# Optimization experiments

Measured on AMD Instinct MI355X. Metric: run time of the kernel, lower is better.

## Reference

```python
import jax, jax.numpy as jnp
import numpy as np

D_MODEL = 1024
N_HEADS = 16
HEAD_DIM = D_MODEL // N_HEADS
NEG_INF = -1e9


def setup_inputs() -> dict:
    key = jax.random.key(0)
    ks = jax.random.split(key, 12)
    B, S = 2, 2048
    std = 1.0 / np.sqrt(D_MODEL)
    def lin(k):
        kw, kb = jax.random.split(k)
        W = jax.random.uniform(kw, (D_MODEL, D_MODEL), jnp.float32, -std, std)
        b = jax.random.uniform(kb, (D_MODEL,), jnp.float32, -std, std)
        return W, b
    Wq, bq = lin(ks[0])
    Wk, bk = lin(ks[1])
    Wv, bv = lin(ks[2])
    Wo, bo = lin(ks[3])
    Q = jax.random.normal(ks[4], (B, S, D_MODEL), jnp.float32)
    K = jax.random.normal(ks[5], (B, S, D_MODEL), jnp.float32)
    V = jax.random.normal(ks[6], (B, S, D_MODEL), jnp.float32)
    # causal attention mask: True means masked (disallowed)
    attn_mask = jnp.triu(jnp.ones((S, S), dtype=bool), k=1)
    padding_mask = jnp.zeros((B, S), dtype=bool)  # no padding
    return {"Q": Q, "K": K, "V": V, "attn_mask": attn_mask,
            "padding_mask": padding_mask,
            "Wq": Wq, "bq": bq, "Wk": Wk, "bk": bk,
            "Wv": Wv, "bv": bv, "Wo": Wo, "bo": bo}


def reference(Q, K, V, attn_mask, padding_mask, Wq, bq, Wk, bk, Wv, bv, Wo, bo):
    B, Sq, _ = Q.shape
    Sk = K.shape[1]
    # QKV projections, split into heads -> [B, H, S, Dh]
    def proj(x, W, b):
        y = x @ W.T + b
        return y.reshape(B, -1, N_HEADS, HEAD_DIM).transpose(0, 2, 1, 3)
    q = proj(Q, Wq, bq)
    k = proj(K, Wk, bk)
    v = proj(V, Wv, bv)
    # scaled dot-product attention (dropout is identity in eval mode)
    scores = jnp.einsum('bhqd,bhkd->bhqk', q, k) / jnp.sqrt(
        jnp.asarray(HEAD_DIM, q.dtype))
    mask = attn_mask[None, None, :, :] | padding_mask[:, None, None, :]
    scores = jnp.where(mask, NEG_INF, scores)
    attn = jax.nn.softmax(scores, axis=-1)
    x = jnp.einsum('bhqk,bhkd->bhqd', attn, v)
    x = x.transpose(0, 2, 1, 3).reshape(B, Sq, D_MODEL)
    return x @ Wo.T + bo
```

## Files before the change

kernel.cpp:

```cpp
#include <hip/hip_runtime.h>
#include <hip/hip_bf16.h>
#include <cstddef>
#include <cstdint>

#define S_LEN  2048
#define DMODEL 1024
#define NHEADS 16

typedef __attribute__((ext_vector_type(8))) short  short8;
typedef __attribute__((ext_vector_type(4))) short  s16x4;
typedef __attribute__((ext_vector_type(8))) __bf16 bf16x8;
typedef __attribute__((ext_vector_type(4))) float  f32x4;

__device__ __forceinline__ f32x4 MFMA(short8 a, short8 b, f32x4 c) {
    return __builtin_amdgcn_mfma_f32_16x16x32_bf16(
        __builtin_bit_cast(bf16x8, a), __builtin_bit_cast(bf16x8, b), c, 0, 0, 0);
}

__device__ __forceinline__ unsigned short f2bs(float f) {
    return __builtin_bit_cast(unsigned short, __float2bfloat16(f));
}
__device__ __forceinline__ float bs2f(unsigned short u) {
    unsigned int x = ((unsigned int)u) << 16;
    return __builtin_bit_cast(float, x);
}

__device__ __forceinline__ short8 cvt8(f32x4 a, f32x4 b) {
    short8 r;
#pragma unroll
    for (int i = 0; i < 4; ++i) {
        r[i]     = (short)f2bs(a[i]);
        r[4 + i] = (short)f2bs(b[i]);
    }
    return r;
}

__device__ __forceinline__ short8 scale8(short8 v) {
    short8 r;
#pragma unroll
    for (int i = 0; i < 8; ++i)
        r[i] = (short)f2bs(bs2f((unsigned short)v[i]) * 0.125f);
    return r;
}

__device__ __forceinline__ int xcd_swz(int bid, int nwg) {
    const int chunk = nwg >> 3;
    return (bid & 7) * chunk + (bid >> 3);
}

template<bool HEADSPLIT>
__device__ __forceinline__ void gemm_body(const void* __restrict__ Ap,
                                          const float* __restrict__ W,
                                          const float* __restrict__ bias,
                                          void* __restrict__ outp,
                                          int m0, int n0)
{
    __shared__ short a_lds[2][128 * 32];
    __shared__ short w_lds[2][128 * 32];
    const int t    = threadIdx.x;
    const int lane = t & 63;
    const int wid  = t >> 6;
    const int wr   = (wid >> 1) << 6;
    const int wc   = (wid & 1) << 6;
    const int fr   = lane & 15;
    const int ks   = lane >> 4;

    const int row0 = t >> 2,         sl0 = t & 3;
    const int row1 = (256 + t) >> 2, sl1 = (256 + t) & 3;
    const int ms0  = sl0 ^ ((row0 >> 1) & 3);
    const int ms1  = sl1 ^ ((row1 >> 1) & 3);

    short8 av_b[2];
    f32x4  av_f[2][2];
    f32x4  wv_f[2][2];

    auto load_tile = [&](int k0) {
        if constexpr (HEADSPLIT) {
            const float* A = (const float*)Ap;
            const float* pa0 = A + (size_t)(m0 + row0) * DMODEL + k0 + sl0 * 8;
            av_f[0][0] = ((const f32x4*)pa0)[0]; av_f[0][1] = ((const f32x4*)pa0)[1];
            const float* pa1 = A + (size_t)(m0 + row1) * DMODEL + k0 + sl1 * 8;
            av_f[1][0] = ((const f32x4*)pa1)[0]; av_f[1][1] = ((const f32x4*)pa1)[1];
        } else {
            const unsigned short* A = (const unsigned short*)Ap;
            av_b[0] = *(const short8*)(A + (size_t)(m0 + row0) * DMODEL + k0 + sl0 * 8);
            av_b[1] = *(const short8*)(A + (size_t)(m0 + row1) * DMODEL + k0 + sl1 * 8);
        }
        const float* pw0 = W + (size_t)(n0 + row0) * DMODEL + k0 + sl0 * 8;
        wv_f[0][0] = ((const f32x4*)pw0)[0]; wv_f[0][1] = ((const f32x4*)pw0)[1];
        const float* pw1 = W + (size_t)(n0 + row1) * DMODEL + k0 + sl1 * 8;
        wv_f[1][0] = ((const f32x4*)pw1)[0]; wv_f[1][1] = ((const f32x4*)pw1)[1];
    };

    auto store_tile = [&](int buf) {
        if constexpr (HEADSPLIT) {
            *(short8*)&a_lds[buf][row0 * 32 + ms0 * 8] = cvt8(av_f[0][0], av_f[0][1]);
            *(short8*)&a_lds[buf][row1 * 32 + ms1 * 8] = cvt8(av_f[1][0], av_f[1][1]);
        } else {
            *(short8*)&a_lds[buf][row0 * 32 + ms0 * 8] = av_b[0];
            *(short8*)&a_lds[buf][row1 * 32 + ms1 * 8] = av_b[1];
        }
        *(short8*)&w_lds[buf][row0 * 32 + ms0 * 8] = cvt8(wv_f[0][0], wv_f[0][1]);
        *(short8*)&w_lds[buf][row1 * 32 + ms1 * 8] = cvt8(wv_f[1][0], wv_f[1][1]);
    };

    load_tile(0);
    store_tile(0);
    load_tile(32);
    __syncthreads();

    f32x4 acc[4][4] = {};

    for (int kidx = 0; kidx < 32; ++kidx) {
        const int cur = kidx & 1;

        short8 af[4], bfr[4];
#pragma unroll
        for (int i = 0; i < 4; ++i) {
            const int ra = wr + i * 16 + fr;
            af[i]  = *(const short8*)&a_lds[cur][ra * 32 + ((ks ^ ((ra >> 1) & 3)) << 3)];
            const int rb = wc + i * 16 + fr;
            bfr[i] = *(const short8*)&w_lds[cur][rb * 32 + ((ks ^ ((rb >> 1) & 3)) << 3)];
        }
        __builtin_amdgcn_s_setprio(1);
#pragma unroll
        for (int mi = 0; mi < 4; ++mi)
#pragma unroll
            for (int ni = 0; ni < 4; ++ni)
                acc[mi][ni] = MFMA(af[mi], bfr[ni], acc[mi][ni]);
        __builtin_amdgcn_s_setprio(0);

        if (kidx + 1 < 32) {
            store_tile(cur ^ 1);
            if (kidx + 2 < 32) load_tile((kidx + 2) * 32);
        }
        __syncthreads();
    }

#pragma unroll
    for (int ni = 0; ni < 4; ++ni) {
        const int n    = n0 + wc + ni * 16 + fr;
        const float bv = bias[n];
#pragma unroll
        for (int mi = 0; mi < 4; ++mi) {
#pragma unroll
            for (int j = 0; j < 4; ++j) {
                const int m = m0 + wr + mi * 16 + ks * 4 + j;
                const float val = acc[mi][ni][j] + bv;
                if constexpr (HEADSPLIT) {
                    const int b = m >> 11, s = m & (S_LEN - 1);
                    const int hh = n >> 6, dh = n & 63;
                    ((unsigned short*)outp)[((((size_t)b * NHEADS + hh) * S_LEN + s) << 6) + dh]
                        = f2bs(val);
                } else {
                    ((float*)outp)[(size_t)m * DMODEL + n] = val;
                }
            }
        }
    }
}

__global__ __launch_bounds__(256, 3)
void qkv_gemm(const float* __restrict__ Q, const float* __restrict__ K,
              const float* __restrict__ V,
              const float* __restrict__ Wq, const float* __restrict__ Wk,
              const float* __restrict__ Wv,
              const float* __restrict__ bq, const float* __restrict__ bk,
              const float* __restrict__ bv,
              unsigned short* qh, unsigned short* kh, unsigned short* vh)
{
    const int swz = xcd_swz(blockIdx.x, 768);
    const int z   = swz >> 8;
    const int rem = swz & 255;
    const int my  = rem >> 3;
    const int nx  = rem & 7;
    const float *A, *W, *B; unsigned short* O;
    if (z == 0)      { A = Q; W = Wq; B = bq; O = qh; }
    else if (z == 1) { A = K; W = Wk; B = bk; O = kh; }
    else             { A = V; W = Wv; B = bv; O = vh; }
    gemm_body<true>(A, W, B, O, my * 128, nx * 128);
}

__global__ __launch_bounds__(256, 3)
void out_gemm(const unsigned short* __restrict__ X, const float* __restrict__ Wo,
              const float* __restrict__ bo, float* __restrict__ out)
{
    const int swz = xcd_swz(blockIdx.x, 256);
    gemm_body<false>(X, Wo, bo, out, (swz >> 3) * 128, (swz & 7) * 128);
}

#define VSTR 72
#define PSTR 88

struct QState {
    short8 qf0, qf1;
    f32x4  oacc[4];
    float  m, l;
    int    qr0;
};

__device__ __forceinline__ void attn_tile(QState& st, const int k0,
                                          const short* k_lds, const short* v_lds,
                                          short* p_buf, const int fr, const int ks)
{
    const int myq = st.qr0 + fr;
    f32x4 sacc[4] = {};
    __builtin_amdgcn_s_setprio(1);
#pragma unroll
    for (int nk = 0; nk < 4; ++nk) {
        const int rb = nk * 16 + fr;
        short8 a0 = *(const short8*)&k_lds[rb * 64 + (((ks)     ^ (rb & 7)) << 3)];
        short8 a1 = *(const short8*)&k_lds[rb * 64 + (((4 + ks) ^ (rb & 7)) << 3)];
        sacc[nk] = MFMA(a0, st.qf0, sacc[nk]);
        sacc[nk] = MFMA(a1, st.qf1, sacc[nk]);
    }
    __builtin_amdgcn_s_setprio(0);

    float mx = -1e9f;
    if (k0 + 63 <= st.qr0) {
#pragma unroll
        for (int nk = 0; nk < 4; ++nk)
#pragma unroll
            for (int jj = 0; jj < 4; ++jj) mx = fmaxf(mx, sacc[nk][jj]);
    } else {
#pragma unroll
        for (int nk = 0; nk < 4; ++nk)
#pragma unroll
            for (int jj = 0; jj < 4; ++jj) {
                const int key = k0 + nk * 16 + ks * 4 + jj;
                float s = (key <= myq) ? sacc[nk][jj] : -1e9f;
                sacc[nk][jj] = s;
                mx = fmaxf(mx, s);
            }
    }
    mx = fmaxf(mx, __shfl_xor(mx, 16));
    mx = fmaxf(mx, __shfl_xor(mx, 32));
    if (!__all(mx <= st.m + 8.f)) {
        const float mnew = fmaxf(st.m, mx);
        const float corr = __expf(st.m - mnew);
        st.m = mnew;
        st.l *= corr;
#pragma unroll
        for (int nd = 0; nd < 4; ++nd)
#pragma unroll
            for (int jj = 0; jj < 4; ++jj) st.oacc[nd][jj] *= corr;
    }

    float rsum = 0.f;
#pragma unroll
    for (int nk = 0; nk < 4; ++nk) {
        s16x4 pw;
#pragma unroll
        for (int jj = 0; jj < 4; ++jj) {
            const float p = __expf(sacc[nk][jj] - st.m);
            rsum += p;
            pw[jj] = (short)f2bs(p);
        }
        *(s16x4*)&p_buf[fr * PSTR + nk * 16 + ks * 4] = pw;
    }
    rsum += __shfl_xor(rsum, 16);
    rsum += __shfl_xor(rsum, 32);
    st.l += rsum;
    asm volatile("" ::: "memory");

    __builtin_amdgcn_s_setprio(1);
#pragma unroll
    for (int sh = 0; sh < 2; ++sh) {
        short8 pa = *(const short8*)&p_buf[fr * PSTR + sh * 32 + ks * 8];
#pragma unroll
        for (int nd = 0; nd < 4; ++nd) {
            short8 vf = *(const short8*)&v_lds[(nd * 16 + fr) * VSTR + sh * 32 + ks * 8];
            st.oacc[nd] = MFMA(vf, pa, st.oacc[nd]);
        }
    }
    __builtin_amdgcn_s_setprio(0);
}

__global__ __launch_bounds__(256, 2)
void attn_kernel(const unsigned short* __restrict__ qh,
                 const unsigned short* __restrict__ kh,
                 const unsigned short* __restrict__ vh,
                 unsigned short* __restrict__ xh)
{
    __shared__ short k_lds[64 * 64];
    __shared__ short v_lds[64 * VSTR];
    __shared__ short p_lds[4][16 * PSTR];

    const int t    = threadIdx.x;
    const int lane = t & 63;
    const int wid  = t >> 6;
    const int fr   = lane & 15;
    const int ks   = lane >> 4;
    const int swz  = xcd_swz(blockIdx.x, 512);
    const int bh   = swz >> 4;
    const int xp   = swz & 15;
    const int qa0  = xp * 64;
    const int qb0  = (31 - xp) * 64;
    const int ntA  = xp + 1;
    const int ntB  = 32 - xp;

    const unsigned short* qb_ = qh + ((size_t)bh << 17);
    const unsigned short* kb  = kh + ((size_t)bh << 17);
    const unsigned short* vb  = vh + ((size_t)bh << 17);

    QState A, B;
    A.qr0 = qa0 + wid * 16;  B.qr0 = qb0 + wid * 16;
    A.qf0 = scale8(*(const short8*)&qb_[(A.qr0 + fr) * 64 + ks * 8]);
    A.qf1 = scale8(*(const short8*)&qb_[(A.qr0 + fr) * 64 + 32 + ks * 8]);
    B.qf0 = scale8(*(const short8*)&qb_[(B.qr0 + fr) * 64 + ks * 8]);
    B.qf1 = scale8(*(const short8*)&qb_[(B.qr0 + fr) * 64 + 32 + ks * 8]);
#pragma unroll
    for (int nd = 0; nd < 4; ++nd) { A.oacc[nd] = f32x4{}; B.oacc[nd] = f32x4{}; }
    A.m = B.m = -1e9f; A.l = B.l = 0.f;

    short8 kv[2], vv[2];
#pragma unroll
    for (int cc = 0; cc < 2; ++cc) {
        const int c   = cc * 256 + t;
        const int row = c >> 3;
        const int sl  = c & 7;
        kv[cc] = *(const short8*)(kb + (size_t)row * 64 + sl * 8);
        const int key = c & 63;
        const int d0  = (c >> 6) * 8;
        vv[cc] = *(const short8*)(vb + (size_t)key * 64 + d0);
    }

    for (int kt = 0; kt < ntB; ++kt) {
        const int k0 = kt * 64;
        __syncthreads();

#pragma unroll
        for (int cc = 0; cc < 2; ++cc) {
            const int c   = cc * 256 + t;
            const int row = c >> 3;
            const int ms  = (c & 7) ^ (row & 7);
            *(short8*)&k_lds[row * 64 + ms * 8] = kv[cc];
            const int key = c & 63;
            const int d0  = (c >> 6) * 8;
#pragma unroll
            for (int i = 0; i < 8; ++i)
                v_lds[(d0 + i) * VSTR + key] = vv[cc][i];
        }
        __syncthreads();

        if (kt + 1 < ntB) {
            const int k1 = k0 + 64;
#pragma unroll
            for (int cc = 0; cc < 2; ++cc) {
                const int c   = cc * 256 + t;
                const int row = c >> 3;
                const int sl  = c & 7;
                kv[cc] = *(const short8*)(kb + (size_t)(k1 + row) * 64 + sl * 8);
                const int key = c & 63;
                const int d0  = (c >> 6) * 8;
                vv[cc] = *(const short8*)(vb + (size_t)(k1 + key) * 64 + d0);
            }
        }

        attn_tile(B, k0, k_lds, v_lds, p_lds[wid], fr, ks);
        if (kt < ntA)
            attn_tile(A, k0, k_lds, v_lds, p_lds[wid], fr, ks);
    }

    const int b = bh >> 4, h = bh & 15;
#pragma unroll
    for (int which = 0; which < 2; ++which) {
        QState& st = which ? B : A;
        const float inv = 1.f / st.l;
        const size_t base = ((size_t)b * S_LEN + (st.qr0 + fr)) * DMODEL + h * 64;
#pragma unroll
        for (int nd = 0; nd < 4; ++nd)
#pragma unroll
            for (int jj = 0; jj < 4; ++jj)
                xh[base + nd * 16 + ks * 4 + jj] = f2bs(st.oacc[nd][jj] * inv);
    }
}

extern "C" void kernel_launch(void* const* d_in, const int* in_sizes, int n_in,
                              void* d_out, int out_size, void* d_ws, size_t ws_size,
                              hipStream_t stream)
{
    const float* Q  = (const float*)d_in[0];
    const float* K  = (const float*)d_in[1];
    const float* V  = (const float*)d_in[2];
    const float* Wq = (const float*)d_in[5];
    const float* bq = (const float*)d_in[6];
    const float* Wk = (const float*)d_in[7];
    const float* bk = (const float*)d_in[8];
    const float* Wv = (const float*)d_in[9];
    const float* bv = (const float*)d_in[10];
    const float* Wo = (const float*)d_in[11];
    const float* bo = (const float*)d_in[12];
    float* out = (float*)d_out;

    const size_t HSZ = (size_t)2 * S_LEN * DMODEL;
    unsigned short* qh = (unsigned short*)d_ws;
    unsigned short* kh = qh + HSZ;
    unsigned short* vh = kh + HSZ;
    unsigned short* xh = vh + HSZ;

    qkv_gemm<<<768, 256, 0, stream>>>(Q, K, V, Wq, Wk, Wv, bq, bk, bv, qh, kh, vh);
    attn_kernel<<<512, 256, 0, stream>>>(qh, kh, vh, xh);
    out_gemm<<<256, 256, 0, stream>>>(xh, Wo, bo, out);
}
```

Baseline: 107.4 us.

## Load GEMM weight fragments directly from global into registers, bypassing LDS

```diff
diff --git a/kernel.cpp b/kernel.cpp
--- a/kernel.cpp
+++ b/kernel.cpp
@@ -56,7 +56,6 @@
                                           int m0, int n0)
 {
     __shared__ short a_lds[2][128 * 32];
-    __shared__ short w_lds[2][128 * 32];
     const int t    = threadIdx.x;
     const int lane = t & 63;
     const int wid  = t >> 6;
@@ -72,9 +71,8 @@
 
     short8 av_b[2];
     f32x4  av_f[2][2];
-    f32x4  wv_f[2][2];
-
-    auto load_tile = [&](int k0) {
+
+    auto load_A = [&](int k0) {
         if constexpr (HEADSPLIT) {
             const float* A = (const float*)Ap;
             const float* pa0 = A + (size_t)(m0 + row0) * DMODEL + k0 + sl0 * 8;
@@ -86,13 +84,8 @@
             av_b[0] = *(const short8*)(A + (size_t)(m0 + row0) * DMODEL + k0 + sl0 * 8);
             av_b[1] = *(const short8*)(A + (size_t)(m0 + row1) * DMODEL + k0 + sl1 * 8);
         }
-        const float* pw0 = W + (size_t)(n0 + row0) * DMODEL + k0 + sl0 * 8;
-        wv_f[0][0] = ((const f32x4*)pw0)[0]; wv_f[0][1] = ((const f32x4*)pw0)[1];
-        const float* pw1 = W + (size_t)(n0 + row1) * DMODEL + k0 + sl1 * 8;
-        wv_f[1][0] = ((const f32x4*)pw1)[0]; wv_f[1][1] = ((const f32x4*)pw1)[1];
     };
-
-    auto store_tile = [&](int buf) {
+    auto store_A = [&](int buf) {
         if constexpr (HEADSPLIT) {
             *(short8*)&a_lds[buf][row0 * 32 + ms0 * 8] = cvt8(av_f[0][0], av_f[0][1]);
             *(short8*)&a_lds[buf][row1 * 32 + ms1 * 8] = cvt8(av_f[1][0], av_f[1][1]);
@@ -100,41 +93,53 @@
             *(short8*)&a_lds[buf][row0 * 32 + ms0 * 8] = av_b[0];
             *(short8*)&a_lds[buf][row1 * 32 + ms1 * 8] = av_b[1];
         }
-        *(short8*)&w_lds[buf][row0 * 32 + ms0 * 8] = cvt8(wv_f[0][0], wv_f[0][1]);
-        *(short8*)&w_lds[buf][row1 * 32 + ms1 * 8] = cvt8(wv_f[1][0], wv_f[1][1]);
     };
 
-    load_tile(0);
-    store_tile(0);
-    load_tile(32);
+    const float* wbase = W + (size_t)(n0 + wc + fr) * DMODEL + ks * 8;
+    auto load_W = [&](int k0, f32x4 (&wf)[4][2]) {
+#pragma unroll
+        for (int ni = 0; ni < 4; ++ni) {
+            const float* p = wbase + (size_t)(ni * 16) * DMODEL + k0;
+            wf[ni][0] = ((const f32x4*)p)[0];
+            wf[ni][1] = ((const f32x4*)p)[1];
+        }
+    };
+
+    load_A(0);
+    store_A(0);
+    load_A(32);
+    f32x4 wfA[4][2], wfB[4][2];
+    load_W(0, wfA);
     __syncthreads();
 
     f32x4 acc[4][4] = {};
 
-    for (int kidx = 0; kidx < 32; ++kidx) {
+    auto step = [&](int kidx, const f32x4 (&wcur)[4][2], f32x4 (&wnxt)[4][2]) {
         const int cur = kidx & 1;
-
         short8 af[4], bfr[4];
 #pragma unroll
         for (int i = 0; i < 4; ++i) {
             const int ra = wr + i * 16 + fr;
-            af[i]  = *(const short8*)&a_lds[cur][ra * 32 + ((ks ^ ((ra >> 1) & 3)) << 3)];
-            const int rb = wc + i * 16 + fr;
-            bfr[i] = *(const short8*)&w_lds[cur][rb * 32 + ((ks ^ ((rb >> 1) & 3)) << 3)];
-        }
-        __builtin_amdgcn_s_setprio(1);
+            af[i] = *(const short8*)&a_lds[cur][ra * 32 + ((ks ^ ((ra >> 1) & 3)) << 3)];
+        }
+#pragma unroll
+        for (int ni = 0; ni < 4; ++ni) bfr[ni] = cvt8(wcur[ni][0], wcur[ni][1]);
+        if (kidx + 1 < 32) load_W((kidx + 1) * 32, wnxt);
 #pragma unroll
         for (int mi = 0; mi < 4; ++mi)
 #pragma unroll
             for (int ni = 0; ni < 4; ++ni)
                 acc[mi][ni] = MFMA(af[mi], bfr[ni], acc[mi][ni]);
-        __builtin_amdgcn_s_setprio(0);
-
         if (kidx + 1 < 32) {
-            store_tile(cur ^ 1);
-            if (kidx + 2 < 32) load_tile((kidx + 2) * 32);
+            store_A(cur ^ 1);
+            if (kidx + 2 < 32) load_A((kidx + 2) * 32);
         }
         __syncthreads();
+    };
+
+    for (int k2 = 0; k2 < 32; k2 += 2) {
+        step(k2,     wfA, wfB);
+        step(k2 + 1, wfB, wfA);
     }
 
 #pragma unroll
```

Result: slower. 215.7 us (+100.7%).
